# Kernel optimization log

Measured on AMD Instinct MI355X. Metric: run time of the kernel, lower is better.

Reference implementation:

```python
import jax, jax.numpy as jnp
import numpy as np

K = 64  # args.gcn_topk


def _gate(W, U, b, x, h, act):
    # torch: act(W.matmul(x) + U.matmul(hidden) + bias), x/h: [B, D, D]
    return act(jnp.einsum('ij,bjk->bik', W, x) + jnp.einsum('ij,bjk->bik', U, h) + b)


def setup_inputs() -> dict:
    key = jax.random.key(0)
    ks = jax.random.split(key, 16)
    B, N, D, R = 8, 4096, 128, 512
    s = 1.0 / np.sqrt(D)
    return {
        'Ahat': jax.random.uniform(ks[0], (B, N, N), dtype=jnp.float32),
        'node_embs': jax.random.normal(ks[1], (B, N, D), dtype=jnp.float32),
        'mask': jnp.zeros((B, N), dtype=jnp.float32),
        'ht': jax.random.normal(ks[2], (B, R), dtype=jnp.float32),
        'prev_Q': jax.random.normal(ks[3], (B, D, D), dtype=jnp.float32),
        'W_map': jax.random.normal(ks[4], (R, D), dtype=jnp.float32) / np.sqrt(R),
        'b_map': jnp.zeros((D,), dtype=jnp.float32),
        'Wu': jax.random.normal(ks[5], (D, D), dtype=jnp.float32) * s,
        'Uu': jax.random.normal(ks[6], (D, D), dtype=jnp.float32) * s,
        'bu': jnp.zeros((D, D), dtype=jnp.float32),
        'Wr': jax.random.normal(ks[7], (D, D), dtype=jnp.float32) * s,
        'Ur': jax.random.normal(ks[8], (D, D), dtype=jnp.float32) * s,
        'br': jnp.zeros((D, D), dtype=jnp.float32),
        'Wh': jax.random.normal(ks[9], (D, D), dtype=jnp.float32) * s,
        'Uh': jax.random.normal(ks[10], (D, D), dtype=jnp.float32) * s,
        'bh': jnp.zeros((D, D), dtype=jnp.float32),
        'static_W': jax.random.normal(ks[11], (D, D), dtype=jnp.float32) * s,
    }


def reference(Ahat, node_embs, mask, ht, prev_Q, W_map, b_map, Wu, Uu, bu,
              Wr, Ur, br, Wh, Uh, bh, static_W):
    B, N, D = node_embs.shape
    # ---- TopK_with_h (ht is detached in torch) ----
    scorer = jnp.tanh(jax.lax.stop_gradient(ht) @ W_map + b_map)            # [B, D]
    scores = jnp.einsum('bnd,bd->bn', node_embs, scorer)                    # [B, N]
    scores = scores / jnp.linalg.norm(scorer, axis=1, keepdims=True)
    vals, topk_idx = jax.lax.top_k(scores, K)                               # [B, K]
    rep = D // K + 1
    idx_rep = jnp.tile(topk_idx, (1, rep))[:, :D]                           # [B, D]
    gathered = jnp.take_along_axis(node_embs, idx_rep[:, :, None], axis=1)  # [B, D, D]
    z = gathered * jnp.tanh(jnp.take_along_axis(scores, idx_rep, axis=1))[:, :, None]
    logp = jax.nn.log_softmax(scores, axis=-1)
    p = jnp.exp(logp)
    entropy = -jnp.sum(p * logp, axis=-1)                                   # [B]
    policy_score = jnp.take_along_axis(logp, idx_rep, axis=1).mean(axis=1)  # [B]
    z_topk = jnp.swapaxes(z, 1, 2)                                          # [B, D, D]
    # ---- mat_GRU_cell: evolve GCN weights ----
    update = _gate(Wu, Uu, bu, z_topk, prev_Q, jax.nn.sigmoid)
    reset = _gate(Wr, Ur, br, z_topk, prev_Q, jax.nn.sigmoid)
    h_cap = _gate(Wh, Uh, bh, z_topk, reset * prev_Q, jnp.tanh)
    new_Q = (1.0 - update) * prev_Q + update * h_cap                        # [B, D, D]
    # ---- pool graph: gather nodes + adjacency rows/cols ----
    ne = jnp.take_along_axis(node_embs, topk_idx[:, :, None], axis=1)       # [B, K, D]
    A = jnp.take_along_axis(Ahat, topk_idx[:, :, None], axis=1)             # [B, K, N]
    A = jnp.take_along_axis(A, topk_idx[:, None, :], axis=2)                # [B, K, K]
    di = jnp.sum(A, axis=1) ** (-0.5)                                       # [B, K]
    A = di[:, None, :] * A * jax.lax.stop_gradient(di)[:, :, None]
    # ---- dual GCN branches (second consumes first, as in torch source) ----
    h1 = jax.nn.relu(A @ (ne @ new_Q))                                      # [B, K, D]
    h2 = jax.nn.relu(A @ (h1 @ static_W))
    out = (h1 + h2) / 2.0
    return out, policy_score, scorer, entropy
```

## Files before the change

kernel.cpp:

```cpp
#include <hip/hip_runtime.h>
#include <cmath>


__device__ __forceinline__ float sigmoidf_(float x){ return 1.0f/(1.0f+expf(-x)); }

__global__ __launch_bounds__(256) void k_scores(const float* __restrict__ node_embs,
    const float* __restrict__ ht, const float* __restrict__ W_map,
    const float* __restrict__ b_map, float* __restrict__ scores,
    float* __restrict__ scorer_out) {
  int blk = blockIdx.x, t = threadIdx.x;
  int b = blk >> 4, part = blk & 15;
  __shared__ float htl[512];
  __shared__ float scn[128];
  __shared__ float red[2];
  for (int e = t; e < 512; e += 256) htl[e] = ht[b*512 + e];
  __syncthreads();
  float scv = 0.f;
  if (t < 128) {
    float acc = b_map[t];
    #pragma unroll 8
    for (int r = 0; r < 512; ++r) acc += htl[r] * W_map[r*128 + t];
    scv = tanhf(acc);
    float ss = scv*scv;
    #pragma unroll
    for (int off = 32; off; off >>= 1) ss += __shfl_xor(ss, off);
    if ((t & 63) == 0) red[t >> 6] = ss;
  }
  __syncthreads();
  float inv = 1.0f / sqrtf(red[0] + red[1]);
  if (t < 128) {
    scn[t] = scv * inv;
    if (part == 0) scorer_out[b*128 + t] = scv;
  }
  __syncthreads();
  int n = part*256 + t;
  const float4* row = (const float4*)(node_embs + ((size_t)(b*4096 + n)) * 128);
  float acc = 0.f;
  #pragma unroll
  for (int j = 0; j < 32; ++j) {
    float4 v = row[j];
    acc += v.x*scn[4*j] + v.y*scn[4*j+1] + v.z*scn[4*j+2] + v.w*scn[4*j+3];
  }
  scores[b*4096 + n] = acc;
}

__global__ __launch_bounds__(256) void k_select(const float* __restrict__ scores,
    const float* __restrict__ node_embs, const float* __restrict__ Ahat,
    float* __restrict__ outPolicy, float* __restrict__ outEntropy,
    int* __restrict__ topk_idx, float* __restrict__ tanhs,
    float* __restrict__ G, float* __restrict__ A_ws) {
  int b = blockIdx.x, t = threadIdx.x;
  int wave = t >> 6, lane = t & 63;
  const float* s = scores + b*4096;

  __shared__ float redf[8];
  __shared__ int   redi[4];
  __shared__ unsigned int candK[256];
  __shared__ int   candI[256];
  __shared__ int   cnt;
  __shared__ int   idxl[64];
  __shared__ float Al[64*65];
  __shared__ float di[64];

  float v[16];
  unsigned int u[16];
  #pragma unroll
  for (int j = 0; j < 16; ++j) {
    float x = s[j*256 + t];
    v[j] = x;
    unsigned int sb = __float_as_uint(x);
    u[j] = (sb & 0x80000000u) ? ~sb : (sb | 0x80000000u);
  }

  float mx = v[0];
  #pragma unroll
  for (int j = 1; j < 16; ++j) mx = fmaxf(mx, v[j]);
  #pragma unroll
  for (int off = 32; off; off >>= 1) mx = fmaxf(mx, __shfl_xor(mx, off));
  if (lane == 0) redf[wave] = mx;
  __syncthreads();
  mx = fmaxf(fmaxf(redf[0], redf[1]), fmaxf(redf[2], redf[3]));
  __syncthreads();
  float S = 0.f, E1 = 0.f;
  #pragma unroll
  for (int j = 0; j < 16; ++j) { float e = expf(v[j] - mx); S += e; E1 += e*(v[j]-mx); }
  #pragma unroll
  for (int off = 32; off; off >>= 1) { S += __shfl_xor(S, off); E1 += __shfl_xor(E1, off); }
  if (lane == 0) { redf[wave] = S; redf[4 + wave] = E1; }
  __syncthreads();
  S  = redf[0] + redf[1] + redf[2] + redf[3];
  E1 = redf[4] + redf[5] + redf[6] + redf[7];
  float logS = logf(S);
  if (t == 0) outEntropy[b] = logS - E1 / S;
  __syncthreads();

  unsigned long long lo = 0ull, hi = 0xFFFFFFFFull;
  for (int it = 0; it < 32; ++it) {
    unsigned long long mid = lo + ((hi - lo + 1ull) >> 1);
    unsigned int midu = (unsigned int)mid;
    int c = 0;
    #pragma unroll
    for (int j = 0; j < 16; ++j) c += (u[j] >= midu) ? 1 : 0;
    #pragma unroll
    for (int off = 32; off; off >>= 1) c += __shfl_xor(c, off);
    if (lane == 0) redi[wave] = c;
    __syncthreads();
    int tot = redi[0] + redi[1] + redi[2] + redi[3];
    __syncthreads();
    if (tot >= 64) lo = mid; else hi = mid - 1ull;
  }
  unsigned int Tstar = (unsigned int)lo;

  if (t == 0) cnt = 0;
  __syncthreads();
  #pragma unroll
  for (int j = 0; j < 16; ++j) {
    if (u[j] >= Tstar) {
      int p = atomicAdd(&cnt, 1);
      if (p < 256) { candK[p] = u[j]; candI[p] = j*256 + t; }
    }
  }
  __syncthreads();
  int nc = cnt < 256 ? cnt : 256;

  if (t < 64) {
    unsigned long long c0 = 0, c1 = 0, c2 = 0, c3 = 0;
    {
      int p;
      p = t;       if (p < nc) c0 = ((unsigned long long)candK[p] << 32) | (unsigned int)(~candI[p]);
      p = 64 + t;  if (p < nc) c1 = ((unsigned long long)candK[p] << 32) | (unsigned int)(~candI[p]);
      p = 128 + t; if (p < nc) c2 = ((unsigned long long)candK[p] << 32) | (unsigned int)(~candI[p]);
      p = 192 + t; if (p < nc) c3 = ((unsigned long long)candK[p] << 32) | (unsigned int)(~candI[p]);
    }
    float vsum = 0.f;
    for (int k = 0; k < 64; ++k) {
      unsigned long long w = c0;
      if (c1 > w) w = c1;
      if (c2 > w) w = c2;
      if (c3 > w) w = c3;
      #pragma unroll
      for (int off = 32; off; off >>= 1) {
        unsigned long long o = __shfl_xor(w, off);
        if (o > w) w = o;
      }
      unsigned int ku = (unsigned int)(w >> 32);
      int wi = (int)(~(unsigned int)(w & 0xFFFFFFFFull));
      if (t == 0) {
        unsigned int sb = (ku & 0x80000000u) ? (ku & 0x7FFFFFFFu) : ~ku;
        float val = __uint_as_float(sb);
        topk_idx[b*64 + k] = wi;
        idxl[k] = wi;
        tanhs[b*64 + k] = tanhf(val);
        vsum += val;
      }
      if (c0 == w) c0 = 0;
      if (c1 == w) c1 = 0;
      if (c2 == w) c2 = 0;
      if (c3 == w) c3 = 0;
    }
    if (t == 0) outPolicy[b] = vsum * (1.0f/64.0f) - mx - logS;
  }
  __syncthreads();

  for (int e = t; e < 8192; e += 256) {
    int k = e >> 7, d = e & 127;
    G[(size_t)b*8192 + e] = node_embs[((size_t)(b*4096 + idxl[k]))*128 + d];
  }

  const float* Ab = Ahat + (size_t)b * 4096 * 4096;
  for (int e = t; e < 4096; e += 256) {
    int p = e >> 6, q = e & 63;
    Al[p*65 + q] = Ab[(size_t)idxl[p]*4096 + idxl[q]];
  }
  __syncthreads();
  if (t < 64) {
    float ssum = 0.f;
    for (int p = 0; p < 64; ++p) ssum += Al[p*65 + t];
    di[t] = 1.0f / sqrtf(ssum);
  }
  __syncthreads();
  for (int e = t; e < 4096; e += 256) {
    int p = e >> 6, q = e & 63;
    A_ws[(size_t)b*4096 + e] = di[p] * di[q] * Al[p*65 + q];
  }
}

__global__ __launch_bounds__(128) void k_gru1(const float* __restrict__ G,
    const float* __restrict__ tanhs, const float* __restrict__ prevQ,
    const float* __restrict__ Wu, const float* __restrict__ Uu, const float* __restrict__ bu,
    const float* __restrict__ Wr, const float* __restrict__ Ur, const float* __restrict__ br,
    float* __restrict__ u_out, float* __restrict__ r_out) {
  int b = blockIdx.x >> 5, i0 = (blockIdx.x & 31) * 4, k = threadIdx.x;
  __shared__ float Gl[64*129];
  __shared__ float Wl[4][128], Ul[4][128], Wrl[4][128], Url[4][128];
  for (int e = k; e < 8192; e += 128) { int rr = e >> 7; Gl[rr*129 + (e & 127)] = G[(size_t)b*8192 + e]; }
  #pragma unroll
  for (int ii = 0; ii < 4; ++ii) {
    Wl[ii][k]  = Wu[(i0+ii)*128 + k]; Ul[ii][k]  = Uu[(i0+ii)*128 + k];
    Wrl[ii][k] = Wr[(i0+ii)*128 + k]; Url[ii][k] = Ur[(i0+ii)*128 + k];
  }
  __syncthreads();
  int km = k & 63;
  float tk = tanhs[b*64 + km];
  const float* Gr = Gl + km*129;
  const float* Q = prevQ + (size_t)b*16384;
  float aW[4] = {0,0,0,0}, aU[4] = {0,0,0,0}, aWr[4] = {0,0,0,0}, aUr[4] = {0,0,0,0};
  for (int j = 0; j < 128; ++j) {
    float g = Gr[j], q = Q[j*128 + k];
    #pragma unroll
    for (int ii = 0; ii < 4; ++ii) {
      aW[ii]  += Wl[ii][j]  * g;  aU[ii]  += Ul[ii][j]  * q;
      aWr[ii] += Wrl[ii][j] * g;  aUr[ii] += Url[ii][j] * q;
    }
  }
  #pragma unroll
  for (int ii = 0; ii < 4; ++ii) {
    int i = i0 + ii; size_t o = ((size_t)b*128 + i)*128 + k;
    u_out[o] = sigmoidf_(aW[ii]*tk  + aU[ii]  + bu[i*128 + k]);
    r_out[o] = sigmoidf_(aWr[ii]*tk + aUr[ii] + br[i*128 + k]);
  }
}

__global__ __launch_bounds__(128) void k_gru2(const float* __restrict__ G,
    const float* __restrict__ tanhs, const float* __restrict__ prevQ,
    const float* __restrict__ Wh, const float* __restrict__ Uh, const float* __restrict__ bh,
    const float* __restrict__ u_ws, const float* __restrict__ r_ws,
    float* __restrict__ Qn) {
  int b = blockIdx.x >> 5, i0 = (blockIdx.x & 31) * 4, k = threadIdx.x;
  __shared__ float Gl[64*129];
  __shared__ float Wl[4][128], Ul[4][128];
  for (int e = k; e < 8192; e += 128) { int rr = e >> 7; Gl[rr*129 + (e & 127)] = G[(size_t)b*8192 + e]; }
  #pragma unroll
  for (int ii = 0; ii < 4; ++ii) {
    Wl[ii][k] = Wh[(i0+ii)*128 + k]; Ul[ii][k] = Uh[(i0+ii)*128 + k];
  }
  __syncthreads();
  int km = k & 63;
  float tk = tanhs[b*64 + km];
  const float* Gr = Gl + km*129;
  const float* Q = prevQ + (size_t)b*16384;
  const float* Rw = r_ws + (size_t)b*16384;
  float aW[4] = {0,0,0,0}, aU[4] = {0,0,0,0};
  for (int j = 0; j < 128; ++j) {
    float g = Gr[j];
    float rq = Rw[j*128 + k] * Q[j*128 + k];
    #pragma unroll
    for (int ii = 0; ii < 4; ++ii) { aW[ii] += Wl[ii][j]*g; aU[ii] += Ul[ii][j]*rq; }
  }
  #pragma unroll
  for (int ii = 0; ii < 4; ++ii) {
    int i = i0 + ii; size_t o = ((size_t)b*128 + i)*128 + k;
    float hc = tanhf(aW[ii]*tk + aU[ii] + bh[i*128 + k]);
    float uu = u_ws[o];
    float qq = Q[i*128 + k];
    Qn[o] = (1.f - uu)*qq + uu*hc;
  }
}

__global__ __launch_bounds__(512) void k_final(const float* __restrict__ G,
    const float* __restrict__ A_ws, const float* __restrict__ Qn,
    const float* __restrict__ Ws, float* __restrict__ out) {
  int b = blockIdx.x, t = threadIdx.x;
  int pg = t >> 7, d = t & 127;
  __shared__ float Al[64*64];
  __shared__ float buf[64*128];
  const float* Gb = G  + (size_t)b*8192;
  const float* Q  = Qn + (size_t)b*16384;
  float* ob = out + (size_t)b*8192;
  for (int e = t; e < 4096; e += 512) Al[e] = A_ws[(size_t)b*4096 + e];
  __syncthreads();

  float acc[16];
  #pragma unroll
  for (int ii = 0; ii < 16; ++ii) acc[ii] = 0.f;
  for (int j = 0; j < 128; ++j) {
    float q = Q[j*128 + d];
    #pragma unroll
    for (int ii = 0; ii < 16; ++ii) acc[ii] += Gb[(pg + ii*4)*128 + j] * q;
  }
  #pragma unroll
  for (int ii = 0; ii < 16; ++ii) buf[(pg + ii*4)*128 + d] = acc[ii];
  __syncthreads();

  float hv[16];
  #pragma unroll
  for (int ii = 0; ii < 16; ++ii) acc[ii] = 0.f;
  for (int q2 = 0; q2 < 64; ++q2) {
    float h0 = buf[q2*128 + d];
    #pragma unroll
    for (int ii = 0; ii < 16; ++ii) acc[ii] += Al[(pg + ii*4)*64 + q2] * h0;
  }
  #pragma unroll
  for (int ii = 0; ii < 16; ++ii) { hv[ii] = fmaxf(acc[ii], 0.f); ob[(pg + ii*4)*128 + d] = hv[ii]; }
  __syncthreads();

  #pragma unroll
  for (int ii = 0; ii < 16; ++ii) acc[ii] = 0.f;
  for (int j = 0; j < 128; ++j) {
    float w = Ws[j*128 + d];
    #pragma unroll
    for (int ii = 0; ii < 16; ++ii) acc[ii] += ob[(pg + ii*4)*128 + j] * w;
  }
  #pragma unroll
  for (int ii = 0; ii < 16; ++ii) buf[(pg + ii*4)*128 + d] = acc[ii];
  __syncthreads();

  #pragma unroll
  for (int ii = 0; ii < 16; ++ii) acc[ii] = 0.f;
  for (int q2 = 0; q2 < 64; ++q2) {
    float mv = buf[q2*128 + d];
    #pragma unroll
    for (int ii = 0; ii < 16; ++ii) acc[ii] += Al[(pg + ii*4)*64 + q2] * mv;
  }
  #pragma unroll
  for (int ii = 0; ii < 16; ++ii)
    ob[(pg + ii*4)*128 + d] = 0.5f * (hv[ii] + fmaxf(acc[ii], 0.f));
}

extern "C" void kernel_launch(void* const* d_in, const int* in_sizes, int n_in,
                              void* d_out, int out_size, void* d_ws, size_t ws_size,
                              hipStream_t stream) {
  const float* Ahat      = (const float*)d_in[0];
  const float* node_embs = (const float*)d_in[1];
  const float* ht        = (const float*)d_in[3];
  const float* prev_Q    = (const float*)d_in[4];
  const float* W_map     = (const float*)d_in[5];
  const float* b_map     = (const float*)d_in[6];
  const float* Wu = (const float*)d_in[7];
  const float* Uu = (const float*)d_in[8];
  const float* bu = (const float*)d_in[9];
  const float* Wr = (const float*)d_in[10];
  const float* Ur = (const float*)d_in[11];
  const float* br = (const float*)d_in[12];
  const float* Wh = (const float*)d_in[13];
  const float* Uh = (const float*)d_in[14];
  const float* bh = (const float*)d_in[15];
  const float* staticW = (const float*)d_in[16];

  float* out = (float*)d_out;
  float* ws  = (float*)d_ws;
  float* scores    = ws;
  int*   topk_idx  = (int*)(ws + 32768);
  float* tanhs     = ws + 33280;
  float* G         = ws + 33792;
  float* u_ws      = ws + 99328;
  float* r_ws      = ws + 230400;
  float* Qn        = ws + 361472;
  float* A_ws      = ws + 492544;

  float* policy  = out + 65536;
  float* scr_out = out + 65544;
  float* entropy = out + 66568;

  k_scores<<<128, 256, 0, stream>>>(node_embs, ht, W_map, b_map, scores, scr_out);
  k_select<<<8, 256, 0, stream>>>(scores, node_embs, Ahat, policy, entropy,
                                  topk_idx, tanhs, G, A_ws);
  k_gru1  <<<256, 128, 0, stream>>>(G, tanhs, prev_Q, Wu, Uu, bu, Wr, Ur, br, u_ws, r_ws);
  k_gru2  <<<256, 128, 0, stream>>>(G, tanhs, prev_Q, Wh, Uh, bh, u_ws, r_ws, Qn);
  k_final <<<8, 512, 0, stream>>>(G, A_ws, Qn, staticW, out);
}
```

Measured before the change: 859.5 us.

## Parallelise scorer matvec, rank-based top-k, stage G and h1 in shared memory

```diff
diff --git a/kernel.cpp b/kernel.cpp
--- a/kernel.cpp
+++ b/kernel.cpp
@@ -11,16 +11,25 @@
   int blk = blockIdx.x, t = threadIdx.x;
   int b = blk >> 4, part = blk & 15;
   __shared__ float htl[512];
+  __shared__ float sp[256];
   __shared__ float scn[128];
   __shared__ float red[2];
   for (int e = t; e < 512; e += 256) htl[e] = ht[b*512 + e];
   __syncthreads();
+  {
+    int col = t & 127, half = t >> 7;
+    const float* Wp = W_map + (size_t)(half*256)*128 + col;
+    const float* hp = htl + half*256;
+    float pacc = 0.f;
+    #pragma unroll 8
+    for (int r = 0; r < 256; ++r) pacc += hp[r] * Wp[(size_t)r*128];
+    sp[t] = pacc;
+  }
+  __syncthreads();
   float scv = 0.f;
   if (t < 128) {
-    float acc = b_map[t];
-    #pragma unroll 8
-    for (int r = 0; r < 512; ++r) acc += htl[r] * W_map[r*128 + t];
-    scv = tanhf(acc);
+    float a = b_map[t] + sp[t] + sp[t + 128];
+    scv = tanhf(a);
     float ss = scv*scv;
     #pragma unroll
     for (int off = 32; off; off >>= 1) ss += __shfl_xor(ss, off);
@@ -59,6 +68,7 @@
   __shared__ int   candI[256];
   __shared__ int   cnt;
   __shared__ int   idxl[64];
+  __shared__ float selV[64];
   __shared__ float Al[64*65];
   __shared__ float di[64];
 
@@ -96,6 +106,7 @@
 
   unsigned long long lo = 0ull, hi = 0xFFFFFFFFull;
   for (int it = 0; it < 32; ++it) {
+    if (lo >= hi) break;
     unsigned long long mid = lo + ((hi - lo + 1ull) >> 1);
     unsigned int midu = (unsigned int)mid;
     int c = 0;
@@ -107,7 +118,10 @@
     __syncthreads();
     int tot = redi[0] + redi[1] + redi[2] + redi[3];
     __syncthreads();
-    if (tot >= 64) lo = mid; else hi = mid - 1ull;
+    bool fin = false;
+    if (tot >= 64) { lo = mid; if (tot == 64) fin = true; }
+    else hi = mid - 1ull;
+    if (fin) break;
   }
   unsigned int Tstar = (unsigned int)lo;
 
@@ -123,44 +137,32 @@
   __syncthreads();
   int nc = cnt < 256 ? cnt : 256;
 
+  if (t < nc) {
+    unsigned long long mykey = ((unsigned long long)candK[t] << 32) | (unsigned int)(~candI[t]);
+    int rank = 0;
+    for (int j = 0; j < nc; ++j) {
+      unsigned long long kj = ((unsigned long long)candK[j] << 32) | (unsigned int)(~candI[j]);
+      rank += (kj > mykey) ? 1 : 0;
+    }
+    if (rank < 64) {
+      unsigned int ku = candK[t];
+      unsigned int sb = (ku & 0x80000000u) ? (ku & 0x7FFFFFFFu) : ~ku;
+      float val = __uint_as_float(sb);
+      int wi = candI[t];
+      topk_idx[b*64 + rank] = wi;
+      idxl[rank] = wi;
+      tanhs[b*64 + rank] = tanhf(val);
+      selV[rank] = val;
+    }
+  }
+  __syncthreads();
+
   if (t < 64) {
-    unsigned long long c0 = 0, c1 = 0, c2 = 0, c3 = 0;
-    {
-      int p;
-      p = t;       if (p < nc) c0 = ((unsigned long long)candK[p] << 32) | (unsigned int)(~candI[p]);
-      p = 64 + t;  if (p < nc) c1 = ((unsigned long long)candK[p] << 32) | (unsigned int)(~candI[p]);
-      p = 128 + t; if (p < nc) c2 = ((unsigned long long)candK[p] << 32) | (unsigned int)(~candI[p]);
-      p = 192 + t; if (p < nc) c3 = ((unsigned long long)candK[p] << 32) | (unsigned int)(~candI[p]);
-    }
-    float vsum = 0.f;
-    for (int k = 0; k < 64; ++k) {
-      unsigned long long w = c0;
-      if (c1 > w) w = c1;
-      if (c2 > w) w = c2;
-      if (c3 > w) w = c3;
-      #pragma unroll
-      for (int off = 32; off; off >>= 1) {
-        unsigned long long o = __shfl_xor(w, off);
-        if (o > w) w = o;
-      }
-      unsigned int ku = (unsigned int)(w >> 32);
-      int wi = (int)(~(unsigned int)(w & 0xFFFFFFFFull));
-      if (t == 0) {
-        unsigned int sb = (ku & 0x80000000u) ? (ku & 0x7FFFFFFFu) : ~ku;
-        float val = __uint_as_float(sb);
-        topk_idx[b*64 + k] = wi;
-        idxl[k] = wi;
-        tanhs[b*64 + k] = tanhf(val);
-        vsum += val;
-      }
-      if (c0 == w) c0 = 0;
-      if (c1 == w) c1 = 0;
-      if (c2 == w) c2 = 0;
-      if (c3 == w) c3 = 0;
-    }
-    if (t == 0) outPolicy[b] = vsum * (1.0f/64.0f) - mx - logS;
-  }
-  __syncthreads();
+    float pv = selV[t];
+    #pragma unroll
+    for (int off = 32; off; off >>= 1) pv += __shfl_xor(pv, off);
+    if (t == 0) outPolicy[b] = pv * (1.0f/64.0f) - mx - logS;
+  }
 
   for (int e = t; e < 8192; e += 256) {
     int k = e >> 7, d = e & 127;
@@ -193,7 +195,13 @@
   int b = blockIdx.x >> 5, i0 = (blockIdx.x & 31) * 4, k = threadIdx.x;
   __shared__ float Gl[64*129];
   __shared__ float Wl[4][128], Ul[4][128], Wrl[4][128], Url[4][128];
-  for (int e = k; e < 8192; e += 128) { int rr = e >> 7; Gl[rr*129 + (e & 127)] = G[(size_t)b*8192 + e]; }
+  const float4* G4 = (const float4*)(G + (size_t)b*8192);
+  for (int e4 = k; e4 < 2048; e4 += 128) {
+    float4 vv = G4[e4];
+    int rr = e4 >> 5, c = (e4 & 31) << 2;
+    float* p = &Gl[rr*129 + c];
+    p[0] = vv.x; p[1] = vv.y; p[2] = vv.z; p[3] = vv.w;
+  }
   #pragma unroll
   for (int ii = 0; ii < 4; ++ii) {
     Wl[ii][k]  = Wu[(i0+ii)*128 + k]; Ul[ii][k]  = Uu[(i0+ii)*128 + k];
@@ -205,6 +213,7 @@
   const float* Gr = Gl + km*129;
   const float* Q = prevQ + (size_t)b*16384;
   float aW[4] = {0,0,0,0}, aU[4] = {0,0,0,0}, aWr[4] = {0,0,0,0}, aUr[4] = {0,0,0,0};
+  #pragma unroll 4
   for (int j = 0; j < 128; ++j) {
     float g = Gr[j], q = Q[j*128 + k];
     #pragma unroll
@@ -229,7 +238,13 @@
   int b = blockIdx.x >> 5, i0 = (blockIdx.x & 31) * 4, k = threadIdx.x;
   __shared__ float Gl[64*129];
   __shared__ float Wl[4][128], Ul[4][128];
-  for (int e = k; e < 8192; e += 128) { int rr = e >> 7; Gl[rr*129 + (e & 127)] = G[(size_t)b*8192 + e]; }
+  const float4* G4 = (const float4*)(G + (size_t)b*8192);
+  for (int e4 = k; e4 < 2048; e4 += 128) {
+    float4 vv = G4[e4];
+    int rr = e4 >> 5, c = (e4 & 31) << 2;
+    float* p = &Gl[rr*129 + c];
+    p[0] = vv.x; p[1] = vv.y; p[2] = vv.z; p[3] = vv.w;
+  }
   #pragma unroll
   for (int ii = 0; ii < 4; ++ii) {
     Wl[ii][k] = Wh[(i0+ii)*128 + k]; Ul[ii][k] = Uh[(i0+ii)*128 + k];
@@ -241,6 +256,7 @@
   const float* Q = prevQ + (size_t)b*16384;
   const float* Rw = r_ws + (size_t)b*16384;
   float aW[4] = {0,0,0,0}, aU[4] = {0,0,0,0};
+  #pragma unroll 4
   for (int j = 0; j < 128; ++j) {
     float g = Gr[j];
     float rq = Rw[j*128 + k] * Q[j*128 + k];
@@ -263,20 +279,28 @@
   int b = blockIdx.x, t = threadIdx.x;
   int pg = t >> 7, d = t & 127;
   __shared__ float Al[64*64];
+  __shared__ float Gs[64*128];
   __shared__ float buf[64*128];
   const float* Gb = G  + (size_t)b*8192;
   const float* Q  = Qn + (size_t)b*16384;
   float* ob = out + (size_t)b*8192;
   for (int e = t; e < 4096; e += 512) Al[e] = A_ws[(size_t)b*4096 + e];
+  for (int e = t; e < 8192; e += 512) Gs[e] = Gb[e];
   __syncthreads();
 
   float acc[16];
   #pragma unroll
   for (int ii = 0; ii < 16; ++ii) acc[ii] = 0.f;
-  for (int j = 0; j < 128; ++j) {
-    float q = Q[j*128 + d];
-    #pragma unroll
-    for (int ii = 0; ii < 16; ++ii) acc[ii] += Gb[(pg + ii*4)*128 + j] * q;
+  for (int j = 0; j < 128; j += 4) {
+    float q0 = Q[(j+0)*128 + d];
+    float q1 = Q[(j+1)*128 + d];
+    float q2 = Q[(j+2)*128 + d];
+    float q3 = Q[(j+3)*128 + d];
+    #pragma unroll
+    for (int ii = 0; ii < 16; ++ii) {
+      float4 g = *(const float4*)&Gs[(pg + ii*4)*128 + j];
+      acc[ii] += g.x*q0 + g.y*q1 + g.z*q2 + g.w*q3;
+    }
   }
   #pragma unroll
   for (int ii = 0; ii < 16; ++ii) buf[(pg + ii*4)*128 + d] = acc[ii];
@@ -291,15 +315,21 @@
     for (int ii = 0; ii < 16; ++ii) acc[ii] += Al[(pg + ii*4)*64 + q2] * h0;
   }
   #pragma unroll
-  for (int ii = 0; ii < 16; ++ii) { hv[ii] = fmaxf(acc[ii], 0.f); ob[(pg + ii*4)*128 + d] = hv[ii]; }
+  for (int ii = 0; ii < 16; ++ii) { hv[ii] = fmaxf(acc[ii], 0.f); Gs[(pg + ii*4)*128 + d] = hv[ii]; }
   __syncthreads();
 
   #pragma unroll
   for (int ii = 0; ii < 16; ++ii) acc[ii] = 0.f;
-  for (int j = 0; j < 128; ++j) {
-    float w = Ws[j*128 + d];
-    #pragma unroll
-    for (int ii = 0; ii < 16; ++ii) acc[ii] += ob[(pg + ii*4)*128 + j] * w;
+  for (int j = 0; j < 128; j += 4) {
+    float w0 = Ws[(j+0)*128 + d];
+    float w1 = Ws[(j+1)*128 + d];
+    float w2 = Ws[(j+2)*128 + d];
+    float w3 = Ws[(j+3)*128 + d];
+    #pragma unroll
+    for (int ii = 0; ii < 16; ++ii) {
+      float4 h = *(const float4*)&Gs[(pg + ii*4)*128 + j];
+      acc[ii] += h.x*w0 + h.y*w1 + h.z*w2 + h.w*w3;
+    }
   }
   #pragma unroll
   for (int ii = 0; ii < 16; ++ii) buf[(pg + ii*4)*128 + d] = acc[ii];
```

Result: faster. 718.5 us (-16.4%).
